# Optimization experiments

Measured on AMD Instinct MI355X. Metric: run time of the kernel, lower is better.

Reference implementation:

```python
import jax, jax.numpy as jnp
import numpy as np
import math

D_MODEL = 1024
NHEAD = 16
D_K = D_MODEL // NHEAD
NUM_LAYERS = 4
D_FF = 4096
SEQ = 2048
BATCH = 1
EPS = 1e-5


def _layer_norm(x, g, b):
    mu = jnp.mean(x, axis=-1, keepdims=True)
    var = jnp.mean((x - mu) ** 2, axis=-1, keepdims=True)
    return (x - mu) * jax.lax.rsqrt(var + EPS) * g + b


def setup_inputs() -> dict:
    key = jax.random.key(0)
    ks = jax.random.split(key, 16)
    s = 0.02
    L, D, F = NUM_LAYERS, D_MODEL, D_FF
    inp = {
        "x": jax.random.normal(ks[0], (BATCH, SEQ, D), dtype=jnp.float32),
        "wq": jax.random.normal(ks[1], (L, D, D), dtype=jnp.float32) * s,
        "bq": jnp.zeros((L, D), dtype=jnp.float32),
        "wk": jax.random.normal(ks[2], (L, D, D), dtype=jnp.float32) * s,
        "bk": jnp.zeros((L, D), dtype=jnp.float32),
        "wv": jax.random.normal(ks[3], (L, D, D), dtype=jnp.float32) * s,
        "bv": jnp.zeros((L, D), dtype=jnp.float32),
        "wo": jax.random.normal(ks[4], (L, D, D), dtype=jnp.float32) * s,
        "bo": jnp.zeros((L, D), dtype=jnp.float32),
        "w1": jax.random.normal(ks[5], (L, D, F), dtype=jnp.float32) * s,
        "b1": jnp.zeros((L, F), dtype=jnp.float32),
        "w2": jax.random.normal(ks[6], (L, F, D), dtype=jnp.float32) * s,
        "b2": jnp.zeros((L, D), dtype=jnp.float32),
        "ln1_g": jnp.ones((L, D), dtype=jnp.float32),
        "ln1_b": jnp.zeros((L, D), dtype=jnp.float32),
        "ln2_g": jnp.ones((L, D), dtype=jnp.float32),
        "ln2_b": jnp.zeros((L, D), dtype=jnp.float32),
    }
    return inp


def _transformer(x, wq, bq, wk, bk, wv, bv, wo, bo, w1, b1, w2, b2,
                 ln1_g, ln1_b, ln2_g, ln2_b):
    B, S, D = x.shape
    scale = math.sqrt(D_K)
    for l in range(NUM_LAYERS):
        # multi-head self-attention (manual QKV matmul + softmax + matmul)
        q = (x @ wq[l] + bq[l]).reshape(B, S, NHEAD, D_K).transpose(0, 2, 1, 3)
        k = (x @ wk[l] + bk[l]).reshape(B, S, NHEAD, D_K).transpose(0, 2, 1, 3)
        v = (x @ wv[l] + bv[l]).reshape(B, S, NHEAD, D_K).transpose(0, 2, 1, 3)
        scores = jnp.einsum('bhqd,bhkd->bhqk', q, k) / scale  # [B,H,S,S]
        attn = jax.nn.softmax(scores, axis=-1)
        ctx = jnp.einsum('bhqk,bhkd->bhqd', attn, v)
        ctx = ctx.transpose(0, 2, 1, 3).reshape(B, S, D)
        attn_out = ctx @ wo[l] + bo[l]
        x = _layer_norm(x + attn_out, ln1_g[l], ln1_b[l])
        # feed-forward network with gelu
        h = jax.nn.gelu(x @ w1[l] + b1[l])
        ffn_out = h @ w2[l] + b2[l]
        x = _layer_norm(x + ffn_out, ln2_g[l], ln2_b[l])
    return x


def reference(x, wq, bq, wk, bk, wv, bv, wo, bo, w1, b1, w2, b2,
              ln1_g, ln1_b, ln2_g, ln2_b):
    return _transformer(x, wq, bq, wk, bk, wv, bv, wo, bo, w1, b1, w2, b2,
                        ln1_g, ln1_b, ln2_g, ln2_b)
```

## Files before the change

kernel.cpp:

```cpp
#include <hip/hip_runtime.h>
#include <hip/hip_bf16.h>
#include <math.h>

typedef __hip_bfloat16 bf16;
typedef __attribute__((ext_vector_type(8))) short bf16x8;
typedef __attribute__((ext_vector_type(4))) float f32x4;

#define EPI_NONE 0
#define EPI_BIAS_BF16 1
#define EPI_BIAS_GELU_BF16 2

#define CLOG 0.18033688f

__device__ __forceinline__ void gload16(const void* g, void* l) {
  __builtin_amdgcn_global_load_lds((const __attribute__((address_space(1))) void*)g,
                                   (__attribute__((address_space(3))) void*)l, 16, 0, 0);
}

__device__ __forceinline__ float gelu_tanh(float x) {
  const float c = 0.7978845608028654f;
  float t = tanhf(c * (x + 0.044715f * x * x * x));
  return 0.5f * x * (1.0f + t);
}

template<int BM, int BN, int BK, int EPI, typename CT>
__global__ __launch_bounds__(256) void gemm_bt(
    const bf16* __restrict__ A, long sAz, int lda,
    const bf16* __restrict__ Bt, long sBz, int ldb,
    CT* __restrict__ C, long sCz, int ldc,
    const float* __restrict__ bias,
    int K, float scale)
{
  constexpr int WM = BM / 2, WN = BN / 2;
  constexpr int MI = WM / 16, NJ = WN / 16;
  constexpr int NA = (BM * BK * 2) / 4096;
  constexpr int NB = (BN * BK * 2) / 4096;
  constexpr int ROWB = BK * 2;
  __shared__ __align__(16) bf16 As[BM * BK];
  __shared__ __align__(16) bf16 Bs[BN * BK];
  const int t = threadIdx.x;
  const int lane = t & 63, w = t >> 6;
  const int wm = (w >> 1) * WM, wn = (w & 1) * WN;
  const int quad = lane >> 4, r16 = lane & 15;
  const long z = blockIdx.z;
  const bf16* Ab = A + z * sAz + (long)blockIdx.y * BM * lda;
  const bf16* Bb = Bt + z * sBz + (long)blockIdx.x * BN * ldb;

  f32x4 acc[MI][NJ];
  #pragma unroll
  for (int i = 0; i < MI; ++i)
    #pragma unroll
    for (int j = 0; j < NJ; ++j)
      acc[i][j] = (f32x4){0.f, 0.f, 0.f, 0.f};

  for (int k0 = 0; k0 < K; k0 += BK) {
    __syncthreads();
    #pragma unroll
    for (int s = 0; s < NA; ++s) {
      int Lb = s * 4096 + t * 16;
      int row = Lb / ROWB, colb = Lb % ROWB;
      gload16((const char*)Ab + (long)row * (lda * 2) + k0 * 2 + colb, (char*)As + Lb);
    }
    #pragma unroll
    for (int s = 0; s < NB; ++s) {
      int Lb = s * 4096 + t * 16;
      int row = Lb / ROWB, colb = Lb % ROWB;
      gload16((const char*)Bb + (long)row * (ldb * 2) + k0 * 2 + colb, (char*)Bs + Lb);
    }
    __syncthreads();

    #pragma unroll
    for (int kk = 0; kk < BK / 32; ++kk) {
      bf16x8 af[MI], bfv[NJ];
      #pragma unroll
      for (int i = 0; i < MI; ++i)
        af[i] = *(const bf16x8*)&As[(wm + i * 16 + r16) * BK + kk * 32 + quad * 8];
      #pragma unroll
      for (int j = 0; j < NJ; ++j)
        bfv[j] = *(const bf16x8*)&Bs[(wn + j * 16 + r16) * BK + kk * 32 + quad * 8];
      #pragma unroll
      for (int i = 0; i < MI; ++i)
        #pragma unroll
        for (int j = 0; j < NJ; ++j)
          acc[i][j] = __builtin_amdgcn_mfma_f32_16x16x32_bf16(af[i], bfv[j], acc[i][j], 0, 0, 0);
    }
  }

  CT* Cb = C + z * sCz;
  #pragma unroll
  for (int i = 0; i < MI; ++i) {
    #pragma unroll
    for (int j = 0; j < NJ; ++j) {
      int col = blockIdx.x * BN + wn + j * 16 + r16;
      float bvv = 0.f;
      if constexpr (EPI == EPI_BIAS_BF16 || EPI == EPI_BIAS_GELU_BF16)
        bvv = bias[col];
      #pragma unroll
      for (int r = 0; r < 4; ++r) {
        long row = (long)blockIdx.y * BM + wm + i * 16 + quad * 4 + r;
        float val = acc[i][j][r] * scale + bvv;
        if constexpr (EPI == EPI_BIAS_GELU_BF16) val = gelu_tanh(val);
        if constexpr (sizeof(CT) == 2)
          Cb[row * (long)ldc + col] = __float2bfloat16(val);
        else
          Cb[row * (long)ldc + col] = val;
      }
    }
  }
}

__global__ __launch_bounds__(256) void flash_attn(
    const bf16* __restrict__ qkv, const bf16* __restrict__ vT,
    float* __restrict__ Osp, float2* __restrict__ ml)
{
  constexpr int SEQ = 2048, LDP = 72;
  __shared__ __align__(16) bf16 Qs[64 * 64];
  __shared__ __align__(16) bf16 Ks[64 * LDP];
  __shared__ __align__(16) bf16 VTs[64 * LDP];
  __shared__ __align__(16) bf16 Ps[64 * LDP];

  const int t = threadIdx.x;
  const int lane = t & 63, w = t >> 6;
  const int quad = lane >> 4, r16 = lane & 15;
  const int wq0 = w * 16;
  const int s0 = blockIdx.x * 64;
  const int h = blockIdx.y;
  const int split = blockIdx.z;
  const int kt0 = split * 16, ktN = kt0 + 16;

  #pragma unroll
  for (int s = 0; s < 2; ++s) {
    int Lb = s * 4096 + t * 16;
    int row = Lb >> 7, colb = Lb & 127;
    int4 v = *(const int4*)(qkv + (long)(s0 + row) * 3072 + h * 64 + (colb >> 1));
    *(int4*)((char*)Qs + Lb) = v;
  }

  const bf16* kp[2]; const bf16* vp[2];
  int krow[2], kcolb[2];
  #pragma unroll
  for (int s = 0; s < 2; ++s) {
    int Lb = s * 4096 + t * 16;
    krow[s] = Lb >> 7; kcolb[s] = Lb & 127;
    kp[s] = qkv + 1024 + (long)h * 64 + (long)krow[s] * 3072 + (kcolb[s] >> 1);
    vp[s] = vT + (long)(h * 64 + krow[s]) * SEQ + (kcolb[s] >> 1);
  }

  int4 rk[2], rv[2];
  #pragma unroll
  for (int s = 0; s < 2; ++s) {
    rk[s] = *(const int4*)(kp[s] + (long)kt0 * 64 * 3072);
    rv[s] = *(const int4*)(vp[s] + (long)kt0 * 64);
  }

  __syncthreads();
  bf16x8 af_q[2];
  #pragma unroll
  for (int kk = 0; kk < 2; ++kk)
    af_q[kk] = *(const bf16x8*)&Qs[(wq0 + r16) * 64 + kk * 32 + quad * 8];

  f32x4 O[4];
  float m_s[4], l_s[4];
  #pragma unroll
  for (int jd = 0; jd < 4; ++jd) O[jd] = (f32x4){0.f, 0.f, 0.f, 0.f};
  #pragma unroll
  for (int r = 0; r < 4; ++r) { m_s[r] = -1e30f; l_s[r] = 0.f; }

  for (int kt = kt0; kt < ktN; ++kt) {
    __syncthreads();
    #pragma unroll
    for (int s = 0; s < 2; ++s) {
      *(int4*)((char*)Ks + (krow[s] * LDP * 2) + kcolb[s]) = rk[s];
      *(int4*)((char*)VTs + (krow[s] * LDP * 2) + kcolb[s]) = rv[s];
    }
    __syncthreads();

    if (kt + 1 < ktN) {
      long k0n = (long)(kt + 1) * 64;
      #pragma unroll
      for (int s = 0; s < 2; ++s) {
        rk[s] = *(const int4*)(kp[s] + k0n * 3072);
        rv[s] = *(const int4*)(vp[s] + k0n);
      }
    }

    f32x4 sc[4];
    #pragma unroll
    for (int j = 0; j < 4; ++j) sc[j] = (f32x4){0.f, 0.f, 0.f, 0.f};
    #pragma unroll
    for (int kk = 0; kk < 2; ++kk) {
      bf16x8 bk_f[4];
      #pragma unroll
      for (int j = 0; j < 4; ++j)
        bk_f[j] = *(const bf16x8*)&Ks[(j * 16 + r16) * LDP + kk * 32 + quad * 8];
      #pragma unroll
      for (int j = 0; j < 4; ++j)
        sc[j] = __builtin_amdgcn_mfma_f32_16x16x32_bf16(af_q[kk], bk_f[j], sc[j], 0, 0, 0);
    }

    #pragma unroll
    for (int r = 0; r < 4; ++r) {
      float mx = fmaxf(fmaxf(sc[0][r], sc[1][r]), fmaxf(sc[2][r], sc[3][r]));
      #pragma unroll
      for (int msk = 1; msk < 16; msk <<= 1)
        mx = fmaxf(mx, __shfl_xor(mx, msk));
      float m_new = fmaxf(m_s[r], mx * CLOG);
      float alpha = exp2f(m_s[r] - m_new);
      m_s[r] = m_new;
      float rs = 0.f;
      #pragma unroll
      for (int j = 0; j < 4; ++j) {
        float pv = exp2f(fmaf(sc[j][r], CLOG, -m_new));
        sc[j][r] = pv;
        rs += pv;
      }
      #pragma unroll
      for (int msk = 1; msk < 16; msk <<= 1)
        rs += __shfl_xor(rs, msk);
      l_s[r] = l_s[r] * alpha + rs;
      #pragma unroll
      for (int jd = 0; jd < 4; ++jd) O[jd][r] *= alpha;
    }

    {
      int prow = wq0 + quad * 4;
      #pragma unroll
      for (int j = 0; j < 4; ++j)
        #pragma unroll
        for (int r = 0; r < 4; ++r)
          Ps[(prow + r) * LDP + j * 16 + r16] = __float2bfloat16(sc[j][r]);
    }
    __syncthreads();

    #pragma unroll
    for (int kk = 0; kk < 2; ++kk) {
      bf16x8 af_p, bv_f[4];
      af_p = *(const bf16x8*)&Ps[(wq0 + r16) * LDP + kk * 32 + quad * 8];
      #pragma unroll
      for (int jd = 0; jd < 4; ++jd)
        bv_f[jd] = *(const bf16x8*)&VTs[(jd * 16 + r16) * LDP + kk * 32 + quad * 8];
      #pragma unroll
      for (int jd = 0; jd < 4; ++jd)
        O[jd] = __builtin_amdgcn_mfma_f32_16x16x32_bf16(af_p, bv_f[jd], O[jd], 0, 0, 0);
    }
  }

  float* Ob = Osp + (long)split * SEQ * 1024;
  #pragma unroll
  for (int r = 0; r < 4; ++r) {
    long row = s0 + wq0 + quad * 4 + r;
    #pragma unroll
    for (int jd = 0; jd < 4; ++jd)
      Ob[row * 1024 + h * 64 + jd * 16 + r16] = O[jd][r];
    if (r16 == 0)
      ml[((long)(split * 16 + h)) * SEQ + row] = make_float2(m_s[r], l_s[r]);
  }
}

__global__ __launch_bounds__(256) void attn_combine(
    const float* __restrict__ Osp, const float2* __restrict__ ml,
    bf16* __restrict__ ctx)
{
  constexpr long SD = 2048L * 1024L;
  const int s = blockIdx.x;
  const int t = threadIdx.x;
  #pragma unroll
  for (int i = 0; i < 4; ++i) {
    int c = t + i * 256;
    int h = c >> 6;
    float2 a = ml[(long)h * 2048 + s];
    float2 b = ml[(long)(16 + h) * 2048 + s];
    float mC = fmaxf(a.x, b.x);
    float w0 = exp2f(a.x - mC), w1 = exp2f(b.x - mC);
    float inv = 1.f / (a.y * w0 + b.y * w1);
    float o = (Osp[(long)s * 1024 + c] * w0 + Osp[SD + (long)s * 1024 + c] * w1) * inv;
    ctx[(long)s * 1024 + c] = __float2bfloat16(o);
  }
}

__global__ __launch_bounds__(256) void transpose_cast(
    const float* __restrict__ in, bf16* __restrict__ out, int R, int C)
{
  __shared__ bf16 tile[32][33];
  const int tx = threadIdx.x, ty = threadIdx.y;
  const int r0 = blockIdx.y * 32, c0 = blockIdx.x * 32;
  #pragma unroll
  for (int d = 0; d < 32; d += 8)
    tile[ty + d][tx] = __float2bfloat16(in[(long)(r0 + ty + d) * C + c0 + tx]);
  __syncthreads();
  #pragma unroll
  for (int d = 0; d < 32; d += 8)
    out[(long)(c0 + ty + d) * R + r0 + tx] = tile[tx][ty + d];
}

__global__ __launch_bounds__(256) void transpose_bf16(
    const bf16* __restrict__ in, bf16* __restrict__ out, int R, int C, int ldin)
{
  __shared__ bf16 tile[32][33];
  const int tx = threadIdx.x, ty = threadIdx.y;
  const int r0 = blockIdx.y * 32, c0 = blockIdx.x * 32;
  #pragma unroll
  for (int d = 0; d < 32; d += 8)
    tile[ty + d][tx] = in[(long)(r0 + ty + d) * ldin + c0 + tx];
  __syncthreads();
  #pragma unroll
  for (int d = 0; d < 32; d += 8)
    out[(long)(c0 + ty + d) * R + r0 + tx] = tile[tx][ty + d];
}

__device__ __forceinline__ float blk_sum(float v, float* sh) {
  #pragma unroll
  for (int o = 32; o > 0; o >>= 1) v += __shfl_down(v, o);
  __syncthreads();
  if ((threadIdx.x & 63) == 0) sh[threadIdx.x >> 6] = v;
  __syncthreads();
  return sh[0] + sh[1] + sh[2] + sh[3];
}

__global__ __launch_bounds__(256) void ln_residual2(
    float* __restrict__ X, const float* __restrict__ d0, const float* __restrict__ d1,
    const float* __restrict__ bias,
    const float* __restrict__ g, const float* __restrict__ b,
    bf16* __restrict__ xb)
{
  __shared__ float sh[4];
  const int t = threadIdx.x;
  const long base = (long)blockIdx.x * 1024;
  float v[4]; float s = 0.f;
  #pragma unroll
  for (int i = 0; i < 4; ++i) {
    int c = t + i * 256;
    float val = X[base + c] + d0[base + c] + d1[base + c] + bias[c];
    v[i] = val; s += val;
  }
  s = blk_sum(s, sh);
  const float mu = s * (1.f / 1024.f);
  float s2 = 0.f;
  #pragma unroll
  for (int i = 0; i < 4; ++i) { float d = v[i] - mu; s2 += d * d; }
  s2 = blk_sum(s2, sh);
  const float rs = rsqrtf(s2 * (1.f / 1024.f) + 1e-5f);
  #pragma unroll
  for (int i = 0; i < 4; ++i) {
    int c = t + i * 256;
    float o = (v[i] - mu) * rs * g[c] + b[c];
    X[base + c] = o;
    xb[base + c] = __float2bfloat16(o);
  }
}

__global__ __launch_bounds__(256) void init_x(
    const float* __restrict__ xin, float* __restrict__ X, bf16* __restrict__ xb, int n)
{
  for (int i = blockIdx.x * 256 + threadIdx.x; i < n; i += gridDim.x * 256) {
    float v = xin[i];
    X[i] = v;
    xb[i] = __float2bfloat16(v);
  }
}

__global__ __launch_bounds__(256) void copy_out(
    const float* __restrict__ X, float* __restrict__ out, int n)
{
  for (int i = blockIdx.x * 256 + threadIdx.x; i < n; i += gridDim.x * 256)
    out[i] = X[i];
}

__global__ __launch_bounds__(256) void concat_bias(
    const float* __restrict__ bq, const float* __restrict__ bk,
    const float* __restrict__ bv, float* __restrict__ out, int n)
{
  for (int i = blockIdx.x * 256 + threadIdx.x; i < n; i += gridDim.x * 256) {
    int l = i / 3072, r = i % 3072;
    int j = r / 1024, c = r % 1024;
    const float* src = (j == 0) ? bq : (j == 1) ? bk : bv;
    out[i] = src[l * 1024 + c];
  }
}

extern "C" void kernel_launch(void* const* d_in, const int* in_sizes, int n_in,
                              void* d_out, int out_size, void* d_ws, size_t ws_size,
                              hipStream_t stream) {
  constexpr int S = 2048, D = 1024, F = 4096, L = 4;
  const float* xin = (const float*)d_in[0];
  const float* wq = (const float*)d_in[1];
  const float* bq = (const float*)d_in[2];
  const float* wk = (const float*)d_in[3];
  const float* bk = (const float*)d_in[4];
  const float* wv = (const float*)d_in[5];
  const float* bvp = (const float*)d_in[6];
  const float* wo = (const float*)d_in[7];
  const float* bo = (const float*)d_in[8];
  const float* w1 = (const float*)d_in[9];
  const float* b1 = (const float*)d_in[10];
  const float* w2 = (const float*)d_in[11];
  const float* b2 = (const float*)d_in[12];
  const float* ln1g = (const float*)d_in[13];
  const float* ln1b = (const float*)d_in[14];
  const float* ln2g = (const float*)d_in[15];
  const float* ln2b = (const float*)d_in[16];

  char* p = (char*)d_ws;
  float* X    = (float*)p; p += (long)S * D * 4;
  float* tmpf = (float*)p; p += 2L * S * D * 4;
  bf16* xb    = (bf16*)p;  p += (long)S * D * 2;
  bf16* qkv   = (bf16*)p;
  bf16* hb    = (bf16*)p;  p += (long)S * 3 * D * 2;
  bf16* ctx   = (bf16*)p;  p += (long)S * D * 2;
  bf16* vT    = (bf16*)p;  p += (long)S * D * 2;
  bf16* wT    = (bf16*)p;  p += (long)F * D * 2;
  float* bias3= (float*)p; p += (long)L * 3 * D * 4;
  float2* ml  = (float2*)p; p += 2L * 16 * S * 8;

  init_x<<<2048, 256, 0, stream>>>(xin, X, xb, S * D);
  concat_bias<<<48, 256, 0, stream>>>(bq, bk, bvp, bias3, L * 3 * D);

  for (int l = 0; l < L; ++l) {
    transpose_cast<<<dim3(D / 32, D / 32), dim3(32, 8), 0, stream>>>(wq + (long)l * D * D, wT, D, D);
    transpose_cast<<<dim3(D / 32, D / 32), dim3(32, 8), 0, stream>>>(wk + (long)l * D * D, wT + (long)D * D, D, D);
    transpose_cast<<<dim3(D / 32, D / 32), dim3(32, 8), 0, stream>>>(wv + (long)l * D * D, wT + 2L * D * D, D, D);
    gemm_bt<128, 128, 64, EPI_BIAS_BF16, bf16><<<dim3(3 * D / 128, S / 128, 1), 256, 0, stream>>>(
        xb, 0L, D, wT, 0L, D, qkv, 0L, 3 * D, bias3 + l * 3 * D, D, 1.f);

    transpose_bf16<<<dim3(D / 32, S / 32), dim3(32, 8), 0, stream>>>(qkv + 2 * D, vT, S, D, 3 * D);

    flash_attn<<<dim3(S / 64, 16, 2), 256, 0, stream>>>(qkv, vT, tmpf, ml);
    attn_combine<<<S, 256, 0, stream>>>(tmpf, ml, ctx);

    transpose_cast<<<dim3(D / 32, D / 32), dim3(32, 8), 0, stream>>>(wo + (long)l * D * D, wT, D, D);
    gemm_bt<128, 64, 64, EPI_NONE, float><<<dim3(D / 64, S / 128, 2), 256, 0, stream>>>(
        ctx, (long)(D / 2), D, wT, (long)(D / 2), D, tmpf, (long)S * D, D, nullptr, D / 2, 1.f);
    ln_residual2<<<S, 256, 0, stream>>>(X, tmpf, tmpf + (long)S * D, bo + l * D,
                                        ln1g + l * D, ln1b + l * D, xb);

    transpose_cast<<<dim3(F / 32, D / 32), dim3(32, 8), 0, stream>>>(w1 + (long)l * D * F, wT, D, F);
    gemm_bt<128, 128, 64, EPI_BIAS_GELU_BF16, bf16><<<dim3(F / 128, S / 128, 1), 256, 0, stream>>>(
        xb, 0L, D, wT, 0L, D, hb, 0L, F, b1 + l * F, D, 1.f);
    transpose_cast<<<dim3(D / 32, F / 32), dim3(32, 8), 0, stream>>>(w2 + (long)l * F * D, wT, F, D);
    gemm_bt<128, 64, 64, EPI_NONE, float><<<dim3(D / 64, S / 128, 2), 256, 0, stream>>>(
        hb, (long)(F / 2), F, wT, (long)(F / 2), F, tmpf, (long)S * D, D, nullptr, F / 2, 1.f);
    ln_residual2<<<S, 256, 0, stream>>>(X, tmpf, tmpf + (long)S * D, b2 + l * D,
                                        ln2g + l * D, ln2b + l * D, xb);
  }
  copy_out<<<2048, 256, 0, stream>>>(X, (float*)d_out, S * D);
}
```

Baseline: 1.206 ms.

## Compute transposed scores in flash attention to cut softmax shuffles and packed P stores

Swaps the MFMA operands so each lane holds scores for one query row across several keys. Row max and sum then need two cross-lane shuffles instead of per-row 16-lane reductions, and each lane keeps one m/l pair. P is written to LDS as packed 4-element vectors with a new row pitch. The per-row alpha is broadcast back into the O accumulator layout with shuffles. The __syncthreads before the PV MFMA is removed because each wave reads only its own P rows, which relies on correct intra-wave ordering of the LDS writes and reads.

```diff
diff --git a/kernel.cpp b/kernel.cpp
--- a/kernel.cpp
+++ b/kernel.cpp
@@ -4,6 +4,7 @@
 
 typedef __hip_bfloat16 bf16;
 typedef __attribute__((ext_vector_type(8))) short bf16x8;
+typedef __attribute__((ext_vector_type(4))) short bf16x4;
 typedef __attribute__((ext_vector_type(4))) float f32x4;
 
 #define EPI_NONE 0
@@ -21,6 +22,11 @@
   const float c = 0.7978845608028654f;
   float t = tanhf(c * (x + 0.044715f * x * x * x));
   return 0.5f * x * (1.0f + t);
+}
+
+__device__ __forceinline__ short bf16bits(float x) {
+  bf16 h = __float2bfloat16(x);
+  return *reinterpret_cast<const short*>(&h);
 }
 
 template<int BM, int BN, int BK, int EPI, typename CT>
@@ -113,11 +119,11 @@
     const bf16* __restrict__ qkv, const bf16* __restrict__ vT,
     float* __restrict__ Osp, float2* __restrict__ ml)
 {
-  constexpr int SEQ = 2048, LDP = 72;
+  constexpr int SEQ = 2048, LDP = 72, LDPP = 80;
   __shared__ __align__(16) bf16 Qs[64 * 64];
   __shared__ __align__(16) bf16 Ks[64 * LDP];
   __shared__ __align__(16) bf16 VTs[64 * LDP];
-  __shared__ __align__(16) bf16 Ps[64 * LDP];
+  __shared__ __align__(16) bf16 Ps[64 * LDPP];
 
   const int t = threadIdx.x;
   const int lane = t & 63, w = t >> 6;
@@ -160,11 +166,9 @@
     af_q[kk] = *(const bf16x8*)&Qs[(wq0 + r16) * 64 + kk * 32 + quad * 8];
 
   f32x4 O[4];
-  float m_s[4], l_s[4];
+  float m_s = -1e30f, l_s = 0.f;
   #pragma unroll
   for (int jd = 0; jd < 4; ++jd) O[jd] = (f32x4){0.f, 0.f, 0.f, 0.f};
-  #pragma unroll
-  for (int r = 0; r < 4; ++r) { m_s[r] = -1e30f; l_s[r] = 0.f; }
 
   for (int kt = kt0; kt < ktN; ++kt) {
     __syncthreads();
@@ -195,47 +199,58 @@
         bk_f[j] = *(const bf16x8*)&Ks[(j * 16 + r16) * LDP + kk * 32 + quad * 8];
       #pragma unroll
       for (int j = 0; j < 4; ++j)
-        sc[j] = __builtin_amdgcn_mfma_f32_16x16x32_bf16(af_q[kk], bk_f[j], sc[j], 0, 0, 0);
-    }
-
-    #pragma unroll
-    for (int r = 0; r < 4; ++r) {
-      float mx = fmaxf(fmaxf(sc[0][r], sc[1][r]), fmaxf(sc[2][r], sc[3][r]));
-      #pragma unroll
-      for (int msk = 1; msk < 16; msk <<= 1)
-        mx = fmaxf(mx, __shfl_xor(mx, msk));
-      float m_new = fmaxf(m_s[r], mx * CLOG);
-      float alpha = exp2f(m_s[r] - m_new);
-      m_s[r] = m_new;
-      float rs = 0.f;
+        sc[j] = __builtin_amdgcn_mfma_f32_16x16x32_bf16(bk_f[j], af_q[kk], sc[j], 0, 0, 0);
+    }
+
+    float mj[4];
+    #pragma unroll
+    for (int j = 0; j < 4; ++j)
+      mj[j] = fmaxf(fmaxf(sc[j][0], sc[j][1]), fmaxf(sc[j][2], sc[j][3]));
+    float mx = fmaxf(fmaxf(mj[0], mj[1]), fmaxf(mj[2], mj[3]));
+    mx = fmaxf(mx, __shfl_xor(mx, 16));
+    mx = fmaxf(mx, __shfl_xor(mx, 32));
+    float m_new = fmaxf(m_s, mx * CLOG);
+    float alpha = exp2f(m_s - m_new);
+    m_s = m_new;
+    float p[4][4], sj[4];
+    #pragma unroll
+    for (int j = 0; j < 4; ++j) {
+      #pragma unroll
+      for (int r = 0; r < 4; ++r)
+        p[j][r] = exp2f(fmaf(sc[j][r], CLOG, -m_new));
+      sj[j] = (p[j][0] + p[j][1]) + (p[j][2] + p[j][3]);
+    }
+    float rs = (sj[0] + sj[1]) + (sj[2] + sj[3]);
+    rs += __shfl_xor(rs, 16);
+    rs += __shfl_xor(rs, 32);
+    l_s = l_s * alpha + rs;
+
+    float ar[4];
+    #pragma unroll
+    for (int r = 0; r < 4; ++r)
+      ar[r] = __shfl(alpha, quad * 20 + r);
+    #pragma unroll
+    for (int jd = 0; jd < 4; ++jd)
+      #pragma unroll
+      for (int r = 0; r < 4; ++r)
+        O[jd][r] *= ar[r];
+
+    {
+      bf16* pr = &Ps[(wq0 + r16) * LDPP + quad * 4];
       #pragma unroll
       for (int j = 0; j < 4; ++j) {
-        float pv = exp2f(fmaf(sc[j][r], CLOG, -m_new));
-        sc[j][r] = pv;
-        rs += pv;
-      }
-      #pragma unroll
-      for (int msk = 1; msk < 16; msk <<= 1)
-        rs += __shfl_xor(rs, msk);
-      l_s[r] = l_s[r] * alpha + rs;
-      #pragma unroll
-      for (int jd = 0; jd < 4; ++jd) O[jd][r] *= alpha;
-    }
-
-    {
-      int prow = wq0 + quad * 4;
-      #pragma unroll
-      for (int j = 0; j < 4; ++j)
+        bf16x4 pk;
         #pragma unroll
         for (int r = 0; r < 4; ++r)
-          Ps[(prow + r) * LDP + j * 16 + r16] = __float2bfloat16(sc[j][r]);
-    }
-    __syncthreads();
+          pk[r] = bf16bits(p[j][r]);
+        *(bf16x4*)(pr + j * 16) = pk;
+      }
+    }
 
     #pragma unroll
     for (int kk = 0; kk < 2; ++kk) {
       bf16x8 af_p, bv_f[4];
-      af_p = *(const bf16x8*)&Ps[(wq0 + r16) * LDP + kk * 32 + quad * 8];
+      af_p = *(const bf16x8*)&Ps[(wq0 + r16) * LDPP + kk * 32 + quad * 8];
       #pragma unroll
       for (int jd = 0; jd < 4; ++jd)
         bv_f[jd] = *(const bf16x8*)&VTs[(jd * 16 + r16) * LDP + kk * 32 + quad * 8];
@@ -252,9 +267,9 @@
     #pragma unroll
     for (int jd = 0; jd < 4; ++jd)
       Ob[row * 1024 + h * 64 + jd * 16 + r16] = O[jd][r];
-    if (r16 == 0)
-      ml[((long)(split * 16 + h)) * SEQ + row] = make_float2(m_s[r], l_s[r]);
-  }
+  }
+  if (quad == 0)
+    ml[((long)(split * 16 + h)) * SEQ + (s0 + wq0 + r16)] = make_float2(m_s, l_s);
 }
 
 __global__ __launch_bounds__(256) void attn_combine(
```

Result: faster. 1.174 ms (-2.7%).
